# Kernel optimization log

Hardware: AMD Instinct MI355X
Metric: run time of the kernel (lower is better)

## Reference

```python
import jax, jax.numpy as jnp
import numpy as np

T1 = 0.2
T2 = 1.2
LABEL_SMOOTHING = 0.05
NUM_ITERS = 20  # fixed-point iterations for lambda_t_a (t2 > 1 branch)


def log_t(x, t):
    # tempered log (t != 1)
    return (x ** (1.0 - t) - 1.0) / (1.0 - t)


def exp_t(x, t):
    # tempered exp (t != 1): relu((1-t)x + 1) ** (1/(1-t))
    return jnp.maximum((1.0 - t) * x + 1.0, 0.0) ** (1.0 / (1.0 - t))


def lambda_t_a(a, t):
    # t > 1 fixed-point branch of the original torch code, with a fixed
    # iteration count instead of a host-synced convergence check.
    mu = jnp.max(a, axis=-1, keepdims=True)            # [N, 1]
    norm_a_initial = a - mu                            # [N, C], <= 0

    def body(norm_a, _):
        z_a = jnp.sum(exp_t(norm_a, t), axis=-1, keepdims=True)  # [N, 1]
        return z_a ** (1.0 - t) * norm_a_initial, None

    norm_a, _ = jax.lax.scan(body, norm_a_initial, None, length=NUM_ITERS)
    z_a = jnp.sum(exp_t(norm_a, t), axis=-1, keepdims=True)
    return -log_t(1.0 / z_a, t) + mu                   # [N, 1]


def setup_inputs() -> dict:
    key = jax.random.key(0)
    k1, k2 = jax.random.split(key)
    N, C = 16384, 1000
    inputs = jax.random.normal(k1, (N, C), dtype=jnp.float32)
    labels = jax.random.randint(k2, (N,), 0, C)
    targets = jax.nn.one_hot(labels, C, dtype=jnp.float32)
    return {"inputs": inputs, "targets": targets}


def reference(inputs, targets):
    num_classes = targets.shape[-1]
    # label smoothing (label_smoothing > 0 branch)
    targets = (1.0 - num_classes / (num_classes - 1) * LABEL_SMOOTHING) * targets \
              + LABEL_SMOOTHING / (num_classes - 1)
    norm_constants = lambda_t_a(inputs, T2)                      # [N, 1]
    probabilities = exp_t(inputs - norm_constants, T2)           # [N, C]
    loss1 = targets * (log_t(targets + 1e-8, T1) - log_t(probabilities, T1))
    loss2 = (targets ** (2.0 - T1) - probabilities ** (2.0 - T1)) / (2.0 - T1)
    out = jnp.sum(loss1 - loss2, axis=-1)                        # [N]
    return jnp.mean(out)
```

## Files before the change

kernel.cpp:

```cpp
#include <hip/hip_runtime.h>
#include <math.h>

#define C_DIM 1000
#define BIG   1.0e30f

__device__ __forceinline__ float fexp2(float x) { return __builtin_amdgcn_exp2f(x); }
__device__ __forceinline__ float flog2(float x) { return __builtin_amdgcn_logf(x); }
__device__ __forceinline__ float frcp(float x)  { return __builtin_amdgcn_rcpf(x); }

__global__ __launch_bounds__(256) void btll(
    const float* __restrict__ inputs, const float* __restrict__ targets,
    float* __restrict__ out, int n_rows, float inv_n,
    float C0, float E_off, float dE)
{
    __shared__ float lds_cap[10240];

    const int lane = threadIdx.x & 63;
    const int wave = threadIdx.x >> 6;
    const int row  = blockIdx.x * 4 + wave;

    float loss = 0.0f;
    if (row < n_rows) {
        const float4* in4 = (const float4*)(inputs  + (size_t)row * C_DIM);
        const float4* tg4 = (const float4*)(targets + (size_t)row * C_DIM);
        const bool m3 = (lane + 192) < 250;

        float4 x0 = in4[lane];
        float4 x1 = in4[lane + 64];
        float4 x2 = in4[lane + 128];
        float4 x3 = m3 ? in4[lane + 192] : make_float4(-BIG, -BIG, -BIG, -BIG);
        float4 t0 = tg4[lane];
        float4 t1 = tg4[lane + 64];
        float4 t2 = tg4[lane + 128];
        float4 t3 = m3 ? tg4[lane + 192] : make_float4(0.f, 0.f, 0.f, 0.f);

        float a[16];
        a[0]=x0.x; a[1]=x0.y; a[2]=x0.z; a[3]=x0.w;
        a[4]=x1.x; a[5]=x1.y; a[6]=x1.z; a[7]=x1.w;
        a[8]=x2.x; a[9]=x2.y; a[10]=x2.z; a[11]=x2.w;
        a[12]=x3.x; a[13]=x3.y; a[14]=x3.z; a[15]=x3.w;

        float ah = 0.0f;
        ah = fmaf(t0.x, a[0], ah);  ah = fmaf(t0.y, a[1], ah);
        ah = fmaf(t0.z, a[2], ah);  ah = fmaf(t0.w, a[3], ah);
        ah = fmaf(t1.x, a[4], ah);  ah = fmaf(t1.y, a[5], ah);
        ah = fmaf(t1.z, a[6], ah);  ah = fmaf(t1.w, a[7], ah);
        ah = fmaf(t2.x, a[8], ah);  ah = fmaf(t2.y, a[9], ah);
        ah = fmaf(t2.z, a[10], ah); ah = fmaf(t2.w, a[11], ah);
        ah = fmaf(t3.x, a[12], ah); ah = fmaf(t3.y, a[13], ah);
        ah = fmaf(t3.z, a[14], ah); ah = fmaf(t3.w, a[15], ah);

        float mu = a[0];
        #pragma unroll
        for (int k = 1; k < 16; ++k) mu = fmaxf(mu, a[k]);
        #pragma unroll
        for (int off = 32; off > 0; off >>= 1) {
            ah += __shfl_xor(ah, off, 64);
            mu  = fmaxf(mu, __shfl_xor(mu, off, 64));
        }

        float b[16];
        #pragma unroll
        for (int k = 0; k < 16; ++k) b[k] = -0.2f * (a[k] - mu);
        const float hb = -0.2f * (ah - mu);

        float s = 0.0f;
        #pragma unroll
        for (int k = 0; k < 16; ++k) {
            float u = 1.0f + b[k];
            float u2 = u * u;
            s += frcp(u2 * u2 * u);
        }
        #pragma unroll
        for (int off = 32; off > 0; off >>= 1) s += __shfl_xor(s, off, 64);
        const float lam = fexp2(-0.2f * flog2(s));

        s = 0.0f;
        #pragma unroll
        for (int k = 0; k < 16; ++k) {
            float u = fmaf(lam, b[k], 1.0f);
            float u2 = u * u;
            s += frcp(u2 * u2 * u);
        }
        #pragma unroll
        for (int off = 32; off > 0; off >>= 1) s += __shfl_xor(s, off, 64);
        float w = fexp2(0.2f * flog2(s));

        {
            float s5 = 0.0f, s6 = 0.0f;
            #pragma unroll
            for (int k = 0; k < 16; ++k) {
                float r  = frcp(w + b[k]);
                float r2 = r * r;
                float r4 = r2 * r2;
                float r5 = r4 * r;
                s5 += r5;
                s6 += r5 * r;
            }
            #pragma unroll
            for (int off = 32; off > 0; off >>= 1) {
                s5 += __shfl_xor(s5, off, 64);
                s6 += __shfl_xor(s6, off, 64);
            }
            w = fmaf((s5 - 1.0f) * 0.2f, frcp(s6), w);
        }

        {
            float S4 = 0.0f, S5 = 0.0f, S6 = 0.0f, S9 = 0.0f, S10 = 0.0f;
            #pragma unroll
            for (int k = 0; k < 16; ++k) {
                float r  = frcp(w + b[k]);
                float r2 = r * r;
                float r4 = r2 * r2;
                float r5 = r4 * r;
                S4  += r4;
                S5  += r5;
                S6  += r5 * r;
                S9  += r4 * r5;
                S10 += r5 * r5;
            }
            #pragma unroll
            for (int off = 32; off > 0; off >>= 1) {
                S4  += __shfl_xor(S4,  off, 64);
                S5  += __shfl_xor(S5,  off, 64);
                S6  += __shfl_xor(S6,  off, 64);
                S9  += __shfl_xor(S9,  off, 64);
                S10 += __shfl_xor(S10, off, 64);
            }
            const float d  = (S5 - 1.0f) * 0.2f * frcp(S6);
            const float w1 = w + d;
            const float S4c = fmaf(-4.0f * d, S5,  S4);
            const float S9c = fmaf(-9.0f * d, S10, S9);
            const float rh  = frcp(w1 + hb);
            const float rh2 = rh * rh;
            const float rh4 = rh2 * rh2;
            loss = fmaf(-E_off, S4c,
                   fmaf(-dE, rh4,
                   fmaf(1.0f / 1.8f, S9c, C0))) * inv_n;
        }
    }

    if (lane == 0) lds_cap[wave] = loss;
    __syncthreads();
    if (threadIdx.x == 0) {
        atomicAdd(out, lds_cap[0] + lds_cap[1] + lds_cap[2] + lds_cap[3]);
    }
}

extern "C" void kernel_launch(void* const* d_in, const int* in_sizes, int n_in,
                              void* d_out, int out_size, void* d_ws, size_t ws_size,
                              hipStream_t stream) {
    const float* inputs  = (const float*)d_in[0];
    const float* targets = (const float*)d_in[1];
    float* out = (float*)d_out;

    const int N = in_sizes[0] / C_DIM;

    const double ls    = 0.05;
    const double c1g_d = 1.0 - (1000.0 / 999.0) * ls;
    const double c2_d  = ls / 999.0;
    const float  tp_on_f  = (float)c1g_d + (float)c2_d;
    const float  tp_off_f = (float)c2_d;
    const double tp_on  = (double)tp_on_f;
    const double tp_off = (double)tp_off_f;
    const double A_on  = (pow(tp_on  + 1e-8, 0.8) - 1.0) / 0.8;
    const double A_off = (pow(tp_off + 1e-8, 0.8) - 1.0) / 0.8;
    const double B_on  = pow(tp_on,  1.8);
    const double B_off = pow(tp_off, 1.8);
    const double E_on_d  = 1.25 * tp_on;
    const double E_off_d = 1.25 * tp_off;
    const double F_on_d  = tp_on  * A_on  + E_on_d  - B_on  / 1.8;
    const double F_off_d = tp_off * A_off + E_off_d - B_off / 1.8;
    const double C0_d    = (C_DIM - 1) * F_off_d + F_on_d;
    const double dE_d    = E_on_d - E_off_d;

    hipMemsetAsync(out, 0, sizeof(float), stream);
    dim3 grid((N + 3) / 4);
    btll<<<grid, 256, 0, stream>>>(inputs, targets, out, N, 1.0f / (float)N,
                                   (float)C0_d, (float)E_off_d, (float)dE_d);
}
```

Measured before the change: 165.3 us.

## Drop a Newton pass, use DPP wave reductions, replace atomics with a reduce kernel

```diff
diff --git a/kernel.cpp b/kernel.cpp
--- a/kernel.cpp
+++ b/kernel.cpp
@@ -8,142 +8,170 @@
 __device__ __forceinline__ float flog2(float x) { return __builtin_amdgcn_logf(x); }
 __device__ __forceinline__ float frcp(float x)  { return __builtin_amdgcn_rcpf(x); }
 
+template <int CTRL, int RM>
+__device__ __forceinline__ float dpp_add_term(float x) {
+    int y = __builtin_amdgcn_update_dpp(0, __float_as_int(x), CTRL, RM, 0xf, true);
+    return __int_as_float(y);
+}
+template <int CTRL, int RM>
+__device__ __forceinline__ float dpp_max_term(float x) {
+    int y = __builtin_amdgcn_update_dpp(__float_as_int(x), __float_as_int(x), CTRL, RM, 0xf, false);
+    return __int_as_float(y);
+}
+
+#define DPP_SUM_CHAIN(x)                      \
+    x += dpp_add_term<0x111, 0xf>(x);         \
+    x += dpp_add_term<0x112, 0xf>(x);         \
+    x += dpp_add_term<0x114, 0xf>(x);         \
+    x += dpp_add_term<0x118, 0xf>(x);         \
+    x += dpp_add_term<0x142, 0xa>(x);         \
+    x += dpp_add_term<0x143, 0xc>(x);
+
+__device__ __forceinline__ float bcast63(float x) {
+    return __int_as_float(__builtin_amdgcn_readlane(__float_as_int(x), 63));
+}
+
+__device__ __forceinline__ float wave_sum(float x) {
+    DPP_SUM_CHAIN(x)
+    return bcast63(x);
+}
+
+__device__ __forceinline__ float wave_max(float x) {
+    x = fmaxf(x, dpp_max_term<0x111, 0xf>(x));
+    x = fmaxf(x, dpp_max_term<0x112, 0xf>(x));
+    x = fmaxf(x, dpp_max_term<0x114, 0xf>(x));
+    x = fmaxf(x, dpp_max_term<0x118, 0xf>(x));
+    x = fmaxf(x, dpp_max_term<0x142, 0xa>(x));
+    x = fmaxf(x, dpp_max_term<0x143, 0xc>(x));
+    return bcast63(x);
+}
+
 __global__ __launch_bounds__(256) void btll(
     const float* __restrict__ inputs, const float* __restrict__ targets,
-    float* __restrict__ out, int n_rows, float inv_n,
+    float* __restrict__ row_out, int n_rows,
     float C0, float E_off, float dE)
 {
-    __shared__ float lds_cap[10240];
-
     const int lane = threadIdx.x & 63;
     const int wave = threadIdx.x >> 6;
     const int row  = blockIdx.x * 4 + wave;
-
-    float loss = 0.0f;
-    if (row < n_rows) {
-        const float4* in4 = (const float4*)(inputs  + (size_t)row * C_DIM);
-        const float4* tg4 = (const float4*)(targets + (size_t)row * C_DIM);
-        const bool m3 = (lane + 192) < 250;
-
-        float4 x0 = in4[lane];
-        float4 x1 = in4[lane + 64];
-        float4 x2 = in4[lane + 128];
-        float4 x3 = m3 ? in4[lane + 192] : make_float4(-BIG, -BIG, -BIG, -BIG);
-        float4 t0 = tg4[lane];
-        float4 t1 = tg4[lane + 64];
-        float4 t2 = tg4[lane + 128];
-        float4 t3 = m3 ? tg4[lane + 192] : make_float4(0.f, 0.f, 0.f, 0.f);
-
-        float a[16];
-        a[0]=x0.x; a[1]=x0.y; a[2]=x0.z; a[3]=x0.w;
-        a[4]=x1.x; a[5]=x1.y; a[6]=x1.z; a[7]=x1.w;
-        a[8]=x2.x; a[9]=x2.y; a[10]=x2.z; a[11]=x2.w;
-        a[12]=x3.x; a[13]=x3.y; a[14]=x3.z; a[15]=x3.w;
-
-        float ah = 0.0f;
-        ah = fmaf(t0.x, a[0], ah);  ah = fmaf(t0.y, a[1], ah);
-        ah = fmaf(t0.z, a[2], ah);  ah = fmaf(t0.w, a[3], ah);
-        ah = fmaf(t1.x, a[4], ah);  ah = fmaf(t1.y, a[5], ah);
-        ah = fmaf(t1.z, a[6], ah);  ah = fmaf(t1.w, a[7], ah);
-        ah = fmaf(t2.x, a[8], ah);  ah = fmaf(t2.y, a[9], ah);
-        ah = fmaf(t2.z, a[10], ah); ah = fmaf(t2.w, a[11], ah);
-        ah = fmaf(t3.x, a[12], ah); ah = fmaf(t3.y, a[13], ah);
-        ah = fmaf(t3.z, a[14], ah); ah = fmaf(t3.w, a[15], ah);
-
-        float mu = a[0];
+    if (row >= n_rows) return;
+
+    const float4* in4 = (const float4*)(inputs  + (size_t)row * C_DIM);
+    const float4* tg4 = (const float4*)(targets + (size_t)row * C_DIM);
+    const bool m3 = (lane + 192) < 250;
+
+    float4 x0 = in4[lane];
+    float4 x1 = in4[lane + 64];
+    float4 x2 = in4[lane + 128];
+    float4 x3 = m3 ? in4[lane + 192] : make_float4(-BIG, -BIG, -BIG, -BIG);
+    float4 t0 = tg4[lane];
+    float4 t1 = tg4[lane + 64];
+    float4 t2 = tg4[lane + 128];
+    float4 t3 = m3 ? tg4[lane + 192] : make_float4(0.f, 0.f, 0.f, 0.f);
+
+    float a[16];
+    a[0]=x0.x; a[1]=x0.y; a[2]=x0.z; a[3]=x0.w;
+    a[4]=x1.x; a[5]=x1.y; a[6]=x1.z; a[7]=x1.w;
+    a[8]=x2.x; a[9]=x2.y; a[10]=x2.z; a[11]=x2.w;
+    a[12]=x3.x; a[13]=x3.y; a[14]=x3.z; a[15]=x3.w;
+
+    float ah = 0.0f;
+    ah = fmaf(t0.x, a[0], ah);  ah = fmaf(t0.y, a[1], ah);
+    ah = fmaf(t0.z, a[2], ah);  ah = fmaf(t0.w, a[3], ah);
+    ah = fmaf(t1.x, a[4], ah);  ah = fmaf(t1.y, a[5], ah);
+    ah = fmaf(t1.z, a[6], ah);  ah = fmaf(t1.w, a[7], ah);
+    ah = fmaf(t2.x, a[8], ah);  ah = fmaf(t2.y, a[9], ah);
+    ah = fmaf(t2.z, a[10], ah); ah = fmaf(t2.w, a[11], ah);
+    ah = fmaf(t3.x, a[12], ah); ah = fmaf(t3.y, a[13], ah);
+    ah = fmaf(t3.z, a[14], ah); ah = fmaf(t3.w, a[15], ah);
+
+    float mu = a[0];
+    #pragma unroll
+    for (int k = 1; k < 16; ++k) mu = fmaxf(mu, a[k]);
+    mu = wave_max(mu);
+    ah = wave_sum(ah);
+
+    float b[16];
+    #pragma unroll
+    for (int k = 0; k < 16; ++k) b[k] = -0.2f * (a[k] - mu);
+    const float hb = -0.2f * (ah - mu);
+
+    float s = 0.0f;
+    #pragma unroll
+    for (int k = 0; k < 16; ++k) {
+        float u = 1.0f + b[k];
+        float u2 = u * u;
+        s += frcp(u2 * u2 * u);
+    }
+    s = wave_sum(s);
+    const float lam = fexp2(-0.2f * flog2(s));
+
+    s = 0.0f;
+    #pragma unroll
+    for (int k = 0; k < 16; ++k) {
+        float u = fmaf(lam, b[k], 1.0f);
+        float u2 = u * u;
+        s += frcp(u2 * u2 * u);
+    }
+    s = wave_sum(s);
+    const float w = fexp2(0.2f * flog2(s));
+
+    float S4 = 0.0f, S5 = 0.0f, S6 = 0.0f, S9 = 0.0f, S10 = 0.0f, S11 = 0.0f;
+    #pragma unroll
+    for (int k = 0; k < 16; ++k) {
+        float r  = frcp(w + b[k]);
+        float r2 = r * r;
+        float r4 = r2 * r2;
+        float r5 = r4 * r;
+        float r9 = r4 * r5;
+        S4  += r4;
+        S5  += r5;
+        S6  += r5 * r;
+        S9  += r9;
+        S10 += r5 * r5;
+        S11 += r9 * r2;
+    }
+    DPP_SUM_CHAIN(S4)
+    DPP_SUM_CHAIN(S5)
+    DPP_SUM_CHAIN(S6)
+    DPP_SUM_CHAIN(S9)
+    DPP_SUM_CHAIN(S10)
+    DPP_SUM_CHAIN(S11)
+    S4 = bcast63(S4);  S5 = bcast63(S5);  S6 = bcast63(S6);
+    S9 = bcast63(S9);  S10 = bcast63(S10); S11 = bcast63(S11);
+
+    const float d   = (S5 - 1.0f) * 0.2f * frcp(S6);
+    const float w1  = w + d;
+    const float d2  = d * d;
+    const float S4c = S4 + fmaf(10.0f * d2, S6,  -4.0f * d * S5);
+    const float S9c = S9 + fmaf(45.0f * d2, S11, -9.0f * d * S10);
+    const float rh  = frcp(w1 + hb);
+    const float rh2 = rh * rh;
+    const float rh4 = rh2 * rh2;
+
+    const float loss = fmaf(-E_off, S4c,
+                       fmaf(-dE, rh4,
+                       fmaf(1.0f / 1.8f, S9c, C0)));
+    if (lane == 0) row_out[row] = loss;
+}
+
+__global__ __launch_bounds__(1024) void reduce_mean(
+    const float* __restrict__ row_out, float* __restrict__ out, int n)
+{
+    __shared__ double sm[16];
+    const int lane = threadIdx.x & 63;
+    const int wv   = threadIdx.x >> 6;
+    double s = 0.0;
+    for (int i = threadIdx.x; i < n; i += 1024) s += (double)row_out[i];
+    #pragma unroll
+    for (int off = 32; off > 0; off >>= 1) s += __shfl_xor(s, off, 64);
+    if (lane == 0) sm[wv] = s;
+    __syncthreads();
+    if (wv == 0) {
+        double t = (lane < 16) ? sm[lane] : 0.0;
         #pragma unroll
-        for (int k = 1; k < 16; ++k) mu = fmaxf(mu, a[k]);
-        #pragma unroll
-        for (int off = 32; off > 0; off >>= 1) {
-            ah += __shfl_xor(ah, off, 64);
-            mu  = fmaxf(mu, __shfl_xor(mu, off, 64));
-        }
-
-        float b[16];
-        #pragma unroll
-        for (int k = 0; k < 16; ++k) b[k] = -0.2f * (a[k] - mu);
-        const float hb = -0.2f * (ah - mu);
-
-        float s = 0.0f;
-        #pragma unroll
-        for (int k = 0; k < 16; ++k) {
-            float u = 1.0f + b[k];
-            float u2 = u * u;
-            s += frcp(u2 * u2 * u);
-        }
-        #pragma unroll
-        for (int off = 32; off > 0; off >>= 1) s += __shfl_xor(s, off, 64);
-        const float lam = fexp2(-0.2f * flog2(s));
-
-        s = 0.0f;
-        #pragma unroll
-        for (int k = 0; k < 16; ++k) {
-            float u = fmaf(lam, b[k], 1.0f);
-            float u2 = u * u;
-            s += frcp(u2 * u2 * u);
-        }
-        #pragma unroll
-        for (int off = 32; off > 0; off >>= 1) s += __shfl_xor(s, off, 64);
-        float w = fexp2(0.2f * flog2(s));
-
-        {
-            float s5 = 0.0f, s6 = 0.0f;
-            #pragma unroll
-            for (int k = 0; k < 16; ++k) {
-                float r  = frcp(w + b[k]);
-                float r2 = r * r;
-                float r4 = r2 * r2;
-                float r5 = r4 * r;
-                s5 += r5;
-                s6 += r5 * r;
-            }
-            #pragma unroll
-            for (int off = 32; off > 0; off >>= 1) {
-                s5 += __shfl_xor(s5, off, 64);
-                s6 += __shfl_xor(s6, off, 64);
-            }
-            w = fmaf((s5 - 1.0f) * 0.2f, frcp(s6), w);
-        }
-
-        {
-            float S4 = 0.0f, S5 = 0.0f, S6 = 0.0f, S9 = 0.0f, S10 = 0.0f;
-            #pragma unroll
-            for (int k = 0; k < 16; ++k) {
-                float r  = frcp(w + b[k]);
-                float r2 = r * r;
-                float r4 = r2 * r2;
-                float r5 = r4 * r;
-                S4  += r4;
-                S5  += r5;
-                S6  += r5 * r;
-                S9  += r4 * r5;
-                S10 += r5 * r5;
-            }
-            #pragma unroll
-            for (int off = 32; off > 0; off >>= 1) {
-                S4  += __shfl_xor(S4,  off, 64);
-                S5  += __shfl_xor(S5,  off, 64);
-                S6  += __shfl_xor(S6,  off, 64);
-                S9  += __shfl_xor(S9,  off, 64);
-                S10 += __shfl_xor(S10, off, 64);
-            }
-            const float d  = (S5 - 1.0f) * 0.2f * frcp(S6);
-            const float w1 = w + d;
-            const float S4c = fmaf(-4.0f * d, S5,  S4);
-            const float S9c = fmaf(-9.0f * d, S10, S9);
-            const float rh  = frcp(w1 + hb);
-            const float rh2 = rh * rh;
-            const float rh4 = rh2 * rh2;
-            loss = fmaf(-E_off, S4c,
-                   fmaf(-dE, rh4,
-                   fmaf(1.0f / 1.8f, S9c, C0))) * inv_n;
-        }
-    }
-
-    if (lane == 0) lds_cap[wave] = loss;
-    __syncthreads();
-    if (threadIdx.x == 0) {
-        atomicAdd(out, lds_cap[0] + lds_cap[1] + lds_cap[2] + lds_cap[3]);
+        for (int off = 32; off > 0; off >>= 1) t += __shfl_xor(t, off, 64);
+        if (lane == 0) out[0] = (float)(t / (double)n);
     }
 }
 
@@ -155,6 +183,7 @@
     float* out = (float*)d_out;
 
     const int N = in_sizes[0] / C_DIM;
+    float* row_out = (float*)d_ws;
 
     const double ls    = 0.05;
     const double c1g_d = 1.0 - (1000.0 / 999.0) * ls;
@@ -174,8 +203,8 @@
     const double C0_d    = (C_DIM - 1) * F_off_d + F_on_d;
     const double dE_d    = E_on_d - E_off_d;
 
-    hipMemsetAsync(out, 0, sizeof(float), stream);
     dim3 grid((N + 3) / 4);
-    btll<<<grid, 256, 0, stream>>>(inputs, targets, out, N, 1.0f / (float)N,
+    btll<<<grid, 256, 0, stream>>>(inputs, targets, row_out, N,
                                    (float)C0_d, (float)E_off_d, (float)dE_d);
-}
+    reduce_mean<<<1, 1024, 0, stream>>>(row_out, out, N);
+}
```

Result: faster. 147.0 us (-11.1%).
